# Performance work log

Hardware: AMD Instinct MI355X
Metric: run time of the kernel (lower is better)

Reference implementation:

```python
import jax, jax.numpy as jnp
import numpy as np

N = 50000        # nodes
E = 800000       # edges (avg degree 16)
C_IN = 128
H = 256          # hidden_channels
C_OUT = 128
DEPTH = 4
K = 2            # k_hops -> K+1 = 3 TAGConv weight matrices
L = DEPTH - 1    # residual layers after layer-0 conv
EPS = 1e-5
SLOPE = 0.01     # LeakyReLU default negative slope


def setup_inputs() -> dict:
    key = jax.random.key(0)
    ks = iter(jax.random.split(key, 24))
    s = 0.02
    x = jax.random.normal(next(ks), (N, C_IN), dtype=jnp.float32)
    edge_index = jax.random.randint(next(ks), (2, E), 0, N, dtype=jnp.int64)
    edge_weight = jax.random.uniform(next(ks), (E,), dtype=jnp.float32)
    return {
        'x': x,
        'edge_index': edge_index,
        'edge_weight': edge_weight,
        'W_emb': jax.random.normal(next(ks), (C_IN, H)) * s,
        'b_emb': jnp.zeros((H,), jnp.float32),
        'conv0_W': jax.random.normal(next(ks), (K + 1, H, H)) * s,
        'conv0_b': jnp.zeros((H,), jnp.float32),
        'norm_g': jnp.ones((L, H), jnp.float32),
        'norm_b': jnp.zeros((L, H), jnp.float32),
        'conv_W': jax.random.normal(next(ks), (L, K + 1, H, H)) * s,
        'conv_b': jnp.zeros((L, H), jnp.float32),
        'mlp_W1': jax.random.normal(next(ks), (L, H, 4 * H)) * s,
        'mlp_b1': jnp.zeros((L, 4 * H), jnp.float32),
        'mlp_g': jnp.ones((L, 4 * H), jnp.float32),
        'mlp_bb': jnp.zeros((L, 4 * H), jnp.float32),
        'mlp_W2': jax.random.normal(next(ks), (L, 4 * H, H)) * s,
        'mlp_b2': jnp.zeros((L, H), jnp.float32),
        'W_out': jax.random.normal(next(ks), (H, C_OUT)) * s,
        'b_out': jnp.zeros((C_OUT,), jnp.float32),
    }


def _bn(h, g, b):
    # BatchNorm1d over node dim (training-mode batch statistics)
    m = h.mean(axis=0)
    v = h.var(axis=0)
    return g * (h - m) * jax.lax.rsqrt(v + EPS) + b


def _tagconv(h, src, dst, ew, Ws, b):
    # TAGConv (normalize=False, no self loops): sum_k (A^k h) W_k + b
    out = h @ Ws[0]
    p = h
    for k in range(1, Ws.shape[0]):
        msg = p[src] * ew[:, None]                      # [E, H] gather
        p = jax.ops.segment_sum(msg, dst, num_segments=h.shape[0])
        out = out + p @ Ws[k]
    return out + b


def reference(x, edge_index, edge_weight, W_emb, b_emb, conv0_W, conv0_b,
              norm_g, norm_b, conv_W, conv_b, mlp_W1, mlp_b1, mlp_g, mlp_bb,
              mlp_W2, mlp_b2, W_out, b_out):
    src, dst = edge_index[0], edge_index[1]
    h = x @ W_emb + b_emb                               # x_embed (t=None)
    h = _tagconv(h, src, dst, edge_weight, conv0_W, conv0_b)  # layer-0 conv only
    for l in range(norm_g.shape[0]):                    # res+ blocks
        z = jax.nn.leaky_relu(_bn(h, norm_g[l], norm_b[l]), SLOPE)
        z = _tagconv(z, src, dst, edge_weight, conv_W[l], conv_b[l])
        # pyg MLP [H, 4H, H]: Linear -> BN -> act -> Linear (plain last)
        z = jax.nn.leaky_relu(_bn(z @ mlp_W1[l] + mlp_b1[l], mlp_g[l], mlp_bb[l]), SLOPE)
        z = z @ mlp_W2[l] + mlp_b2[l]
        h = h + z                                       # residual (res=Identity)
    return h @ W_out + b_out
```

## Files before the change

### kernel.cpp

```cpp
#include <hip/hip_runtime.h>

#define HDIM 256
#define EPSV 1e-5f
#define SLOPEV 0.01f

typedef __bf16 bf16;
typedef bf16  bf16x8 __attribute__((ext_vector_type(8)));
typedef bf16  bf16x4 __attribute__((ext_vector_type(4)));
typedef float f32x4  __attribute__((ext_vector_type(4)));

#define GLD16(g, l) __builtin_amdgcn_global_load_lds( \
    (const __attribute__((address_space(1))) void*)(g), \
    (__attribute__((address_space(3))) void*)(l), 16, 0, 0)

template<bool STORE_BF16>
__global__ __launch_bounds__(256)
void gemm_bt_k(const bf16* A0, const bf16* A1, const bf16* A2, const bf16* A3,
               int nseg, int segK,
               const bf16* __restrict__ Wt,
               const float* __restrict__ bias, const bf16* __restrict__ addb,
               void* out0, void* out1, void* out2, void* out3, int ldo,
               int n_store, float* part, int n_stats)
{
    __shared__ char smem[32768];
    bf16* As = (bf16*)smem;
    bf16* Bs = (bf16*)(smem + 16384);

    const int tid = threadIdx.x;
    const int wave = tid >> 6, lane = tid & 63;
    const int quad = lane >> 4, l16 = lane & 15;
    const int waveM = (wave >> 1) * 64, waveN = (wave & 1) * 64;
    const int bm = blockIdx.y * 128, bn = blockIdx.x * 128;
    const int K = nseg * segK;

    const bf16* segs[4] = {A0, A1, A2, A3};
    const int srow = tid >> 3;
    const int skof = (tid & 7) * 8;
    char* lA = (char*)As + wave * 1024;
    char* lB = (char*)Bs + wave * 1024;
    const bf16* pa = As + (waveM + l16) * 64 + quad * 8;
    const bf16* pb = Bs + (waveN + l16) * 64 + quad * 8;

    f32x4 acc[4][4] = {};

    for (int s = 0; s < nseg; ++s) {
        const bf16* gA = segs[s] + (size_t)(bm + srow) * segK + skof;
        const bf16* gB = Wt + (size_t)(bn + srow) * K + s * segK + skof;
        const size_t offA = (size_t)32 * segK;
        const size_t offB = (size_t)32 * K;
        for (int kt = 0; kt < segK; kt += 64) {
            GLD16(gA,            lA);
            GLD16(gA + offA,     lA + 4096);
            GLD16(gA + 2 * offA, lA + 8192);
            GLD16(gA + 3 * offA, lA + 12288);
            GLD16(gB,            lB);
            GLD16(gB + offB,     lB + 4096);
            GLD16(gB + 2 * offB, lB + 8192);
            GLD16(gB + 3 * offB, lB + 12288);
            gA += 64; gB += 64;
            __syncthreads();

#pragma unroll
            for (int ks = 0; ks < 2; ++ks) {
                const bf16* pak = pa + ks * 32;
                const bf16* pbk = pb + ks * 32;
                bf16x8 a0 = *(const bf16x8*)(pak);
                bf16x8 a1 = *(const bf16x8*)(pak + 16 * 64);
                bf16x8 a2 = *(const bf16x8*)(pak + 32 * 64);
                bf16x8 a3 = *(const bf16x8*)(pak + 48 * 64);
                bf16x8 b0 = *(const bf16x8*)(pbk);
                bf16x8 b1 = *(const bf16x8*)(pbk + 16 * 64);
                bf16x8 b2 = *(const bf16x8*)(pbk + 32 * 64);
                bf16x8 b3 = *(const bf16x8*)(pbk + 48 * 64);

                acc[0][0] = __builtin_amdgcn_mfma_f32_16x16x32_bf16(a0, b0, acc[0][0], 0, 0, 0);
                acc[0][1] = __builtin_amdgcn_mfma_f32_16x16x32_bf16(a0, b1, acc[0][1], 0, 0, 0);
                acc[0][2] = __builtin_amdgcn_mfma_f32_16x16x32_bf16(a0, b2, acc[0][2], 0, 0, 0);
                acc[0][3] = __builtin_amdgcn_mfma_f32_16x16x32_bf16(a0, b3, acc[0][3], 0, 0, 0);
                acc[1][0] = __builtin_amdgcn_mfma_f32_16x16x32_bf16(a1, b0, acc[1][0], 0, 0, 0);
                acc[1][1] = __builtin_amdgcn_mfma_f32_16x16x32_bf16(a1, b1, acc[1][1], 0, 0, 0);
                acc[1][2] = __builtin_amdgcn_mfma_f32_16x16x32_bf16(a1, b2, acc[1][2], 0, 0, 0);
                acc[1][3] = __builtin_amdgcn_mfma_f32_16x16x32_bf16(a1, b3, acc[1][3], 0, 0, 0);
                acc[2][0] = __builtin_amdgcn_mfma_f32_16x16x32_bf16(a2, b0, acc[2][0], 0, 0, 0);
                acc[2][1] = __builtin_amdgcn_mfma_f32_16x16x32_bf16(a2, b1, acc[2][1], 0, 0, 0);
                acc[2][2] = __builtin_amdgcn_mfma_f32_16x16x32_bf16(a2, b2, acc[2][2], 0, 0, 0);
                acc[2][3] = __builtin_amdgcn_mfma_f32_16x16x32_bf16(a2, b3, acc[2][3], 0, 0, 0);
                acc[3][0] = __builtin_amdgcn_mfma_f32_16x16x32_bf16(a3, b0, acc[3][0], 0, 0, 0);
                acc[3][1] = __builtin_amdgcn_mfma_f32_16x16x32_bf16(a3, b1, acc[3][1], 0, 0, 0);
                acc[3][2] = __builtin_amdgcn_mfma_f32_16x16x32_bf16(a3, b2, acc[3][2], 0, 0, 0);
                acc[3][3] = __builtin_amdgcn_mfma_f32_16x16x32_bf16(a3, b3, acc[3][3], 0, 0, 0);
            }
            __syncthreads();
        }
    }

    float bv[4];
#pragma unroll
    for (int j = 0; j < 4; ++j)
        bv[j] = bias ? bias[bn + waveN + j * 16 + l16] : 0.f;
#pragma unroll
    for (int i = 0; i < 4; ++i)
#pragma unroll
        for (int j = 0; j < 4; ++j)
#pragma unroll
            for (int r = 0; r < 4; ++r)
                acc[i][j][r] += bv[j];

    void* outs[4] = {out0, out1, out2, out3};

    if (STORE_BF16) {
        char* stg = smem + wave * 4352;
        float s8[8] = {}, q8[8] = {};
        const int rsel = lane >> 3, csel = lane & 7;
#pragma unroll
        for (int ih = 0; ih < 2; ++ih) {
            __syncthreads();
#pragma unroll
            for (int iw = 0; iw < 2; ++iw) {
                int i = ih * 2 + iw;
#pragma unroll
                for (int j = 0; j < 4; ++j)
#pragma unroll
                    for (int r = 0; r < 4; ++r)
                        *(bf16*)(stg + ((iw * 16 + quad * 4 + r) * 68 + j * 16 + l16) * 2)
                            = (bf16)acc[i][j][r];
            }
            __syncthreads();
#pragma unroll
            for (int rr = 0; rr < 4; ++rr) {
                int rl = rsel + rr * 8;
                bf16x4 lo = *(const bf16x4*)(stg + (rl * 68 + csel * 8) * 2);
                bf16x4 hi = *(const bf16x4*)(stg + (rl * 68 + csel * 8 + 4) * 2);
                int rowg = bm + waveM + ih * 32 + rl;
                int colg = bn + waveN + csel * 8;
                int cseg = colg >> 8, cloc = colg & 255;
                size_t idx = (size_t)rowg * ldo + cloc;
                float f[8];
#pragma unroll
                for (int u = 0; u < 4; ++u) { f[u] = (float)lo[u]; f[4 + u] = (float)hi[u]; }
                if (addb) {
                    bf16x8 o = *(const bf16x8*)(addb + idx);
#pragma unroll
                    for (int u = 0; u < 8; ++u) f[u] += (float)o[u];
                }
                bf16x8 w;
#pragma unroll
                for (int u = 0; u < 8; ++u) w[u] = (bf16)f[u];
                if (rowg < n_store) *(bf16x8*)((bf16*)outs[cseg] + idx) = w;
                if (part && rowg < n_stats) {
#pragma unroll
                    for (int u = 0; u < 8; ++u) { s8[u] += f[u]; q8[u] += f[u] * f[u]; }
                }
            }
        }
        if (part) {
#pragma unroll
            for (int m = 8; m <= 32; m <<= 1)
#pragma unroll
                for (int u = 0; u < 8; ++u) {
                    s8[u] += __shfl_xor(s8[u], m, 64);
                    q8[u] += __shfl_xor(q8[u], m, 64);
                }
            __syncthreads();
            float* Ls = (float*)smem;
            float* Lq = Ls + 256;
            if (rsel == 0) {
#pragma unroll
                for (int u = 0; u < 8; ++u) {
                    Ls[wave * 64 + csel * 8 + u] = s8[u];
                    Lq[wave * 64 + csel * 8 + u] = q8[u];
                }
            }
            __syncthreads();
            if (tid < 128) {
                int hi = tid >> 6, c6 = tid & 63;
                float s = Ls[hi * 64 + c6] + Ls[(hi + 2) * 64 + c6];
                float q = Lq[hi * 64 + c6] + Lq[(hi + 2) * 64 + c6];
                int Mtot = gridDim.x * 128;
                int colg = bn + tid;
                part[(size_t)blockIdx.y * Mtot + colg] = s;
                part[(size_t)(gridDim.y + blockIdx.y) * Mtot + colg] = q;
            }
        }
    } else {
#pragma unroll
        for (int i = 0; i < 4; ++i)
#pragma unroll
            for (int j = 0; j < 4; ++j) {
                int colg = bn + waveN + j * 16 + l16;
                int cseg = colg >> 8, cloc = colg & 255;
#pragma unroll
                for (int r = 0; r < 4; ++r) {
                    int rowg = bm + waveM + i * 16 + quad * 4 + r;
                    if (rowg < n_store)
                        ((float*)outs[cseg])[(size_t)rowg * ldo + cloc] = acc[i][j][r];
                }
            }
    }
}

__global__ __launch_bounds__(256)
void finalize_k(const float* __restrict__ part, int GY, int M,
                const float* __restrict__ g, const float* __restrict__ bb,
                float* __restrict__ coef, float invn)
{
    const int c = blockIdx.x;
    const int t = threadIdx.x;
    float s = 0.f, q = 0.f;
    const float* ps = part + c;
    const float* pq = part + (size_t)GY * M + c;
    for (int i = t; i < GY; i += 256) {
        s += ps[(size_t)i * M];
        q += pq[(size_t)i * M];
    }
#pragma unroll
    for (int m = 1; m <= 32; m <<= 1) {
        s += __shfl_xor(s, m, 64);
        q += __shfl_xor(q, m, 64);
    }
    __shared__ float Ls[4], Lq[4];
    const int w = t >> 6, l = t & 63;
    if (l == 0) { Ls[w] = s; Lq[w] = q; }
    __syncthreads();
    if (t == 0) {
        s = Ls[0] + Ls[1] + Ls[2] + Ls[3];
        q = Lq[0] + Lq[1] + Lq[2] + Lq[3];
        float mean = s * invn;
        float var  = q * invn - mean * mean;
        float a = g[c] * rsqrtf(var + EPSV);
        coef[c]     = a;
        coef[M + c] = bb[c] - mean * a;
    }
}

__global__ __launch_bounds__(256)
void transpose_cvt_k(const float* __restrict__ src, bf16* __restrict__ dst,
                     int Kseg, int M, int G)
{
    __shared__ float t[32][33];
    const int z = blockIdx.z;
    src += (size_t)z * Kseg * M;
    const int ldd = G * Kseg;
    dst += (size_t)(z / G) * M * ldd + (size_t)(z % G) * Kseg;
    const int tM = blockIdx.x * 32, tK = blockIdx.y * 32;
    const int tx = threadIdx.x & 31, ty = threadIdx.x >> 5;
#pragma unroll
    for (int r = 0; r < 4; ++r)
        t[ty + r * 8][tx] = src[(size_t)(tK + ty + r * 8) * M + tM + tx];
    __syncthreads();
#pragma unroll
    for (int r = 0; r < 4; ++r)
        dst[(size_t)(tM + ty + r * 8) * ldd + tK + tx] = (bf16)t[tx][ty + r * 8];
}

__global__ __launch_bounds__(256)
void cvt_bf_k(const float* __restrict__ src, bf16* __restrict__ dst, long n4)
{
    long i = (long)blockIdx.x * blockDim.x + threadIdx.x;
    if (i >= n4) return;
    float4 v = ((const float4*)src)[i];
    bf16x4 o; o[0] = (bf16)v.x; o[1] = (bf16)v.y; o[2] = (bf16)v.z; o[3] = (bf16)v.w;
    ((bf16x4*)dst)[i] = o;
}

__global__ __launch_bounds__(256)
void deg_k(const int* __restrict__ dst, int* __restrict__ deg, int E)
{
    int e = blockIdx.x * blockDim.x + threadIdx.x;
    if (e < E) atomicAdd(&deg[dst[e]], 1);
}

__global__ __launch_bounds__(256)
void blocksum_k(const int* __restrict__ deg, int* __restrict__ bsum, int N)
{
    int i = blockIdx.x * 256 + threadIdx.x;
    int v = (i < N) ? deg[i] : 0;
#pragma unroll
    for (int m = 1; m <= 32; m <<= 1) v += __shfl_xor(v, m, 64);
    __shared__ int Ls[4];
    if ((threadIdx.x & 63) == 0) Ls[threadIdx.x >> 6] = v;
    __syncthreads();
    if (threadIdx.x == 0) bsum[blockIdx.x] = Ls[0] + Ls[1] + Ls[2] + Ls[3];
}

__global__ __launch_bounds__(256)
void topscan_k(const int* __restrict__ bsum, int* __restrict__ boff, int nb)
{
    __shared__ int s[256];
    int t = threadIdx.x;
    int v = (t < nb) ? bsum[t] : 0;
    s[t] = v;
    __syncthreads();
    for (int off = 1; off < 256; off <<= 1) {
        int u = (t >= off) ? s[t - off] : 0;
        __syncthreads();
        s[t] += u;
        __syncthreads();
    }
    if (t < nb) boff[t] = s[t] - v;
}

__global__ __launch_bounds__(256)
void scatterscan_k(int* __restrict__ deg_wp, const int* __restrict__ boff,
                   int* __restrict__ rowptr, int N)
{
    __shared__ int s[256];
    int t = threadIdx.x;
    int i = blockIdx.x * 256 + t;
    int v = (i < N) ? deg_wp[i] : 0;
    s[t] = v;
    __syncthreads();
    for (int off = 1; off < 256; off <<= 1) {
        int u = (t >= off) ? s[t - off] : 0;
        __syncthreads();
        s[t] += u;
        __syncthreads();
    }
    if (i < N) {
        int incl = s[t] + boff[blockIdx.x];
        rowptr[i + 1] = incl;
        deg_wp[i] = incl - v;
        if (i == 0) rowptr[0] = 0;
    }
}

__global__ __launch_bounds__(256)
void reorder_k(const int* __restrict__ src, const int* __restrict__ dst,
               const float* __restrict__ ew, int* __restrict__ wp,
               int* __restrict__ col, float* __restrict__ wgt, int E)
{
    int e = blockIdx.x * blockDim.x + threadIdx.x;
    if (e >= E) return;
    int d = dst[e];
    int pos = atomicAdd(&wp[d], 1);
    col[pos] = src[e];
    wgt[pos] = ew[e];
}

__global__ __launch_bounds__(256)
void spmm_pull_k(const bf16* __restrict__ P, const int* __restrict__ rowptr,
                 const int* __restrict__ col, const float* __restrict__ wgt,
                 bf16* __restrict__ Q, int N)
{
    int node = blockIdx.x * 8 + (threadIdx.x >> 5);
    int l = threadIdx.x & 31;
    if (node >= N) return;
    int e = rowptr[node], end = rowptr[node + 1];
    float acc[8] = {};
    for (; e + 1 < end; e += 2) {
        int   s0 = col[e], s1 = col[e + 1];
        float w0 = wgt[e], w1 = wgt[e + 1];
        bf16x8 v0 = *(const bf16x8*)(P + (size_t)s0 * HDIM + l * 8);
        bf16x8 v1 = *(const bf16x8*)(P + (size_t)s1 * HDIM + l * 8);
#pragma unroll
        for (int u = 0; u < 8; ++u)
            acc[u] += (float)v0[u] * w0 + (float)v1[u] * w1;
    }
    if (e < end) {
        int s0 = col[e]; float w0 = wgt[e];
        bf16x8 v0 = *(const bf16x8*)(P + (size_t)s0 * HDIM + l * 8);
#pragma unroll
        for (int u = 0; u < 8; ++u) acc[u] += (float)v0[u] * w0;
    }
    bf16x8 o;
#pragma unroll
    for (int u = 0; u < 8; ++u) o[u] = (bf16)acc[u];
    *(bf16x8*)(Q + (size_t)node * HDIM + l * 8) = o;
}

__global__ __launch_bounds__(256)
void apply_bn_k(const bf16* __restrict__ X, const float* __restrict__ coef,
                bf16* __restrict__ Y, int n)
{
    __shared__ float aL[256], bL[256];
    const int tid = threadIdx.x;
    aL[tid] = coef[tid]; bL[tid] = coef[256 + tid];
    __syncthreads();
    long n4 = (long)n * 64;
    for (long i = (long)blockIdx.x * 256 + tid; i < n4; i += (long)gridDim.x * 256) {
        bf16x4 v = ((const bf16x4*)X)[i];
        int c4 = (int)(i & 63) * 4;
        float r0 = fmaf((float)v[0], aL[c4 + 0], bL[c4 + 0]); r0 = r0 > 0.f ? r0 : SLOPEV * r0;
        float r1 = fmaf((float)v[1], aL[c4 + 1], bL[c4 + 1]); r1 = r1 > 0.f ? r1 : SLOPEV * r1;
        float r2 = fmaf((float)v[2], aL[c4 + 2], bL[c4 + 2]); r2 = r2 > 0.f ? r2 : SLOPEV * r2;
        float r3 = fmaf((float)v[3], aL[c4 + 3], bL[c4 + 3]); r3 = r3 > 0.f ? r3 : SLOPEV * r3;
        bf16x4 o; o[0] = (bf16)r0; o[1] = (bf16)r1; o[2] = (bf16)r2; o[3] = (bf16)r3;
        ((bf16x4*)Y)[i] = o;
    }
}

__global__ __launch_bounds__(256)
void apply_bn4_k(bf16* X0, bf16* X1, bf16* X2, bf16* X3,
                 const float* __restrict__ coef, int n)
{
    __shared__ float aL[1024], bL[1024];
    const int tid = threadIdx.x;
#pragma unroll
    for (int q = 0; q < 4; ++q) {
        int c = q * 256 + tid;
        aL[c] = coef[c]; bL[c] = coef[1024 + c];
    }
    __syncthreads();
    bf16* Xs[4] = {X0, X1, X2, X3};
    long per = (long)n * 64;
    long stride = (long)gridDim.x * 256;
    for (int q = 0; q < 4; ++q) {
        bf16* X = Xs[q];
        int cbase = q * 256;
        for (long i = (long)blockIdx.x * 256 + tid; i < per; i += stride) {
            bf16x4 v = ((const bf16x4*)X)[i];
            int c4 = cbase + (int)(i & 63) * 4;
            float r0 = fmaf((float)v[0], aL[c4 + 0], bL[c4 + 0]); r0 = r0 > 0.f ? r0 : SLOPEV * r0;
            float r1 = fmaf((float)v[1], aL[c4 + 1], bL[c4 + 1]); r1 = r1 > 0.f ? r1 : SLOPEV * r1;
            float r2 = fmaf((float)v[2], aL[c4 + 2], bL[c4 + 2]); r2 = r2 > 0.f ? r2 : SLOPEV * r2;
            float r3 = fmaf((float)v[3], aL[c4 + 3], bL[c4 + 3]); r3 = r3 > 0.f ? r3 : SLOPEV * r3;
            bf16x4 o; o[0] = (bf16)r0; o[1] = (bf16)r1; o[2] = (bf16)r2; o[3] = (bf16)r3;
            ((bf16x4*)X)[i] = o;
        }
    }
}

struct GemmArgs {
    const bf16 *A0, *A1, *A2, *A3; int nseg, segK;
    const bf16* Wt; const float* bias; const bf16* addb;
    void *o0, *o1, *o2, *o3; int ldo, M, n_store;
    float* part; int n_stats;
};

static void gemm(hipStream_t st, const GemmArgs& a, int GY, bool store_bf16)
{
    dim3 g(a.M / 128, GY), b(256);
    if (store_bf16)
        gemm_bt_k<true><<<g, b, 0, st>>>(a.A0, a.A1, a.A2, a.A3, a.nseg, a.segK,
            a.Wt, a.bias, a.addb, a.o0, a.o1, a.o2, a.o3, a.ldo, a.n_store,
            a.part, a.n_stats);
    else
        gemm_bt_k<false><<<g, b, 0, st>>>(a.A0, a.A1, a.A2, a.A3, a.nseg, a.segK,
            a.Wt, a.bias, a.addb, a.o0, a.o1, a.o2, a.o3, a.ldo, a.n_store,
            a.part, a.n_stats);
}

extern "C" void kernel_launch(void* const* d_in, const int* in_sizes, int n_in,
                              void* d_out, int out_size, void* d_ws, size_t ws_size,
                              hipStream_t stream)
{
    const float* x       = (const float*)d_in[0];
    const int*   ei      = (const int*)d_in[1];
    const float* ew      = (const float*)d_in[2];
    const float* W_emb   = (const float*)d_in[3];
    const float* b_emb   = (const float*)d_in[4];
    const float* conv0_W = (const float*)d_in[5];
    const float* conv0_b = (const float*)d_in[6];
    const float* norm_g  = (const float*)d_in[7];
    const float* norm_b  = (const float*)d_in[8];
    const float* conv_W  = (const float*)d_in[9];
    const float* conv_b  = (const float*)d_in[10];
    const float* mlp_W1  = (const float*)d_in[11];
    const float* mlp_b1  = (const float*)d_in[12];
    const float* mlp_g   = (const float*)d_in[13];
    const float* mlp_bb  = (const float*)d_in[14];
    const float* mlp_W2  = (const float*)d_in[15];
    const float* mlp_b2  = (const float*)d_in[16];
    const float* W_out   = (const float*)d_in[17];
    const float* b_out   = (const float*)d_in[18];

    const int N = in_sizes[0] / 128;
    const int E = in_sizes[2];
    const int* srcI = ei;
    const int* dstI = ei + E;
    const int N_pad = ((N + 127) / 128) * 128;
    const int GY = N_pad / 128;
    const int NB = (N + 255) / 256;

    const size_t NHp = (size_t)N_pad * HDIM;
    bf16* xb = (bf16*)d_ws;
    bf16* hb = xb + (size_t)N_pad * 128;
    bf16* cb = hb + NHp;
    bf16* p1 = cb + NHp;
    bf16* p2 = p1 + NHp;
    bf16* e1 = p2 + NHp;
    bf16* e2 = e1 + NHp;
    bf16* wa = e2 + NHp;
    bf16* Wt_emb   = wa;
    bf16* Wt_conv0 = wa + 32768;
    bf16* Wt_conv  = wa + 229376;
    bf16* Wt_mlp1  = wa + 819200;
    bf16* Wt_mlp2  = wa + 1605632;
    bf16* Wt_out   = wa + 2392064;
    float* cf_h   = (float*)(wa + 2424832);
    float* cf_m   = cf_h + 512;
    float* partb  = cf_m + 2048;
    int*   rowptr = (int*)(partb + 2 * (size_t)GY * 1024);
    int*   wp     = rowptr + (N + 1);
    int*   col    = wp + N;
    float* wgt    = (float*)(col + E);
    int*   bsum   = (int*)(wgt + E);
    int*   boff   = bsum + 256;

    const float invn = 1.0f / (float)N;
    dim3 pg((N + 7) / 8), pb(256);

    hipMemsetAsync(wp, 0, (size_t)N * 4, stream);
    deg_k<<<dim3((E + 255) / 256), dim3(256), 0, stream>>>(dstI, wp, E);
    blocksum_k<<<dim3(NB), dim3(256), 0, stream>>>(wp, bsum, N);
    topscan_k<<<dim3(1), dim3(256), 0, stream>>>(bsum, boff, NB);
    scatterscan_k<<<dim3(NB), dim3(256), 0, stream>>>(wp, boff, rowptr, N);
    reorder_k<<<dim3((E + 255) / 256), dim3(256), 0, stream>>>(srcI, dstI, ew, wp, col, wgt, E);

    cvt_bf_k<<<dim3((N * 32 + 255) / 256), dim3(256), 0, stream>>>(x, xb, (long)N * 32);
    transpose_cvt_k<<<dim3(8, 4, 1), dim3(256), 0, stream>>>(W_emb, Wt_emb, 128, 256, 1);
    transpose_cvt_k<<<dim3(8, 8, 3), dim3(256), 0, stream>>>(conv0_W, Wt_conv0, 256, 256, 3);
    transpose_cvt_k<<<dim3(8, 8, 9), dim3(256), 0, stream>>>(conv_W, Wt_conv, 256, 256, 3);
    transpose_cvt_k<<<dim3(32, 8, 3), dim3(256), 0, stream>>>(mlp_W1, Wt_mlp1, 256, 1024, 1);
    transpose_cvt_k<<<dim3(8, 32, 3), dim3(256), 0, stream>>>(mlp_W2, Wt_mlp2, 1024, 256, 1);
    transpose_cvt_k<<<dim3(4, 8, 1), dim3(256), 0, stream>>>(W_out, Wt_out, 256, 128, 1);

    {
        GemmArgs a{xb, xb, xb, xb, 1, 128, Wt_emb, b_emb, nullptr,
                   cb, cb, cb, cb, HDIM, 256, N_pad, nullptr, 0};
        gemm(stream, a, GY, true);
    }

    spmm_pull_k<<<pg, pb, 0, stream>>>(cb, rowptr, col, wgt, p1, N);
    spmm_pull_k<<<pg, pb, 0, stream>>>(p1, rowptr, col, wgt, p2, N);
    {
        GemmArgs a{cb, p1, p2, p2, 3, 256, Wt_conv0, conv0_b, nullptr,
                   hb, hb, hb, hb, HDIM, 256, N_pad, partb, N};
        gemm(stream, a, GY, true);
    }
    finalize_k<<<dim3(256), dim3(256), 0, stream>>>(partb, GY, 256, norm_g, norm_b, cf_h, invn);

    for (int l = 0; l < 3; ++l) {
        apply_bn_k<<<dim3(1024), dim3(256), 0, stream>>>(hb, cf_h, e1, N);

        spmm_pull_k<<<pg, pb, 0, stream>>>(e1, rowptr, col, wgt, p1, N);
        spmm_pull_k<<<pg, pb, 0, stream>>>(p1, rowptr, col, wgt, p2, N);
        {
            GemmArgs a{e1, p1, p2, p2, 3, 256, Wt_conv + (size_t)l * 196608,
                       conv_b + l * 256, nullptr, cb, cb, cb, cb, HDIM, 256, N_pad,
                       nullptr, 0};
            gemm(stream, a, GY, true);
        }

        {
            GemmArgs a{cb, cb, cb, cb, 1, 256, Wt_mlp1 + (size_t)l * 262144,
                       mlp_b1 + (size_t)l * 1024, nullptr, p1, p2, e1, e2, HDIM, 1024,
                       N_pad, partb, N};
            gemm(stream, a, GY, true);
        }
        finalize_k<<<dim3(1024), dim3(256), 0, stream>>>(partb, GY, 1024,
                                                         mlp_g + (size_t)l * 1024,
                                                         mlp_bb + (size_t)l * 1024, cf_m, invn);

        apply_bn4_k<<<dim3(2048), dim3(256), 0, stream>>>(p1, p2, e1, e2, cf_m, N);

        {
            GemmArgs a{p1, p2, e1, e2, 4, 256, Wt_mlp2 + (size_t)l * 262144,
                       mlp_b2 + l * 256, hb, hb, hb, hb, hb, HDIM, 256, N_pad,
                       (l < 2) ? partb : nullptr, N};
            gemm(stream, a, GY, true);
        }
        if (l < 2)
            finalize_k<<<dim3(256), dim3(256), 0, stream>>>(partb, GY, 256,
                                                            norm_g + (l + 1) * 256,
                                                            norm_b + (l + 1) * 256, cf_h, invn);
    }

    {
        GemmArgs a{hb, hb, hb, hb, 1, 256, Wt_out, b_out, nullptr,
                   d_out, d_out, d_out, d_out, 128, 128, N, nullptr, 0};
        gemm(stream, a, GY, false);
    }
}
```

Before: 1.494 ms.

## Double-buffer GEMM LDS tiles with K=32 steps and XCD-aware block remap

Restructures the GEMM main loop from a single-buffered K=64 tile into a double-buffered K=32 pipeline. The next tile's global-to-LDS loads are issued before computing on the current one, and each iteration has one barrier instead of two. Blocks are also remapped so consecutive tiles land on the same XCD chiplet for better L2 reuse. The intent is to hide load latency behind MFMA work, at the cost of smaller per-iteration compute and more loop overhead.

Measured after the change: 1.394 ms. -6.7%, faster.

```diff
diff --git a/kernel.cpp b/kernel.cpp
--- a/kernel.cpp
+++ b/kernel.cpp
@@ -23,75 +23,85 @@
                int n_store, float* part, int n_stats)
 {
     __shared__ char smem[32768];
-    bf16* As = (bf16*)smem;
-    bf16* Bs = (bf16*)(smem + 16384);
 
     const int tid = threadIdx.x;
     const int wave = tid >> 6, lane = tid & 63;
     const int quad = lane >> 4, l16 = lane & 15;
     const int waveM = (wave >> 1) * 64, waveN = (wave & 1) * 64;
-    const int bm = blockIdx.y * 128, bn = blockIdx.x * 128;
+
+    int bid = blockIdx.y * gridDim.x + blockIdx.x;
+    const int nwg = gridDim.x * gridDim.y;
+    if ((nwg & 7) == 0) {
+        const int cpx = nwg >> 3;
+        bid = (bid & 7) * cpx + (bid >> 3);
+    }
+    const int bx = bid % gridDim.x, by = bid / gridDim.x;
+    const int bm = by * 128, bn = bx * 128;
     const int K = nseg * segK;
 
     const bf16* segs[4] = {A0, A1, A2, A3};
-    const int srow = tid >> 3;
-    const int skof = (tid & 7) * 8;
-    char* lA = (char*)As + wave * 1024;
-    char* lB = (char*)Bs + wave * 1024;
-    const bf16* pa = As + (waveM + l16) * 64 + quad * 8;
-    const bf16* pb = Bs + (waveN + l16) * 64 + quad * 8;
+    const int srow = tid >> 2;
+    const int skof = (tid & 3) * 8;
+    char* lAw = smem + wave * 1024;
+    char* lBw = smem + 16384 + wave * 1024;
 
     f32x4 acc[4][4] = {};
 
-    for (int s = 0; s < nseg; ++s) {
-        const bf16* gA = segs[s] + (size_t)(bm + srow) * segK + skof;
-        const bf16* gB = Wt + (size_t)(bn + srow) * K + s * segK + skof;
-        const size_t offA = (size_t)32 * segK;
-        const size_t offB = (size_t)32 * K;
-        for (int kt = 0; kt < segK; kt += 64) {
-            GLD16(gA,            lA);
-            GLD16(gA + offA,     lA + 4096);
-            GLD16(gA + 2 * offA, lA + 8192);
-            GLD16(gA + 3 * offA, lA + 12288);
-            GLD16(gB,            lB);
-            GLD16(gB + offB,     lB + 4096);
-            GLD16(gB + 2 * offB, lB + 8192);
-            GLD16(gB + 3 * offB, lB + 12288);
-            gA += 64; gB += 64;
-            __syncthreads();
-
-#pragma unroll
-            for (int ks = 0; ks < 2; ++ks) {
-                const bf16* pak = pa + ks * 32;
-                const bf16* pbk = pb + ks * 32;
-                bf16x8 a0 = *(const bf16x8*)(pak);
-                bf16x8 a1 = *(const bf16x8*)(pak + 16 * 64);
-                bf16x8 a2 = *(const bf16x8*)(pak + 32 * 64);
-                bf16x8 a3 = *(const bf16x8*)(pak + 48 * 64);
-                bf16x8 b0 = *(const bf16x8*)(pbk);
-                bf16x8 b1 = *(const bf16x8*)(pbk + 16 * 64);
-                bf16x8 b2 = *(const bf16x8*)(pbk + 32 * 64);
-                bf16x8 b3 = *(const bf16x8*)(pbk + 48 * 64);
-
-                acc[0][0] = __builtin_amdgcn_mfma_f32_16x16x32_bf16(a0, b0, acc[0][0], 0, 0, 0);
-                acc[0][1] = __builtin_amdgcn_mfma_f32_16x16x32_bf16(a0, b1, acc[0][1], 0, 0, 0);
-                acc[0][2] = __builtin_amdgcn_mfma_f32_16x16x32_bf16(a0, b2, acc[0][2], 0, 0, 0);
-                acc[0][3] = __builtin_amdgcn_mfma_f32_16x16x32_bf16(a0, b3, acc[0][3], 0, 0, 0);
-                acc[1][0] = __builtin_amdgcn_mfma_f32_16x16x32_bf16(a1, b0, acc[1][0], 0, 0, 0);
-                acc[1][1] = __builtin_amdgcn_mfma_f32_16x16x32_bf16(a1, b1, acc[1][1], 0, 0, 0);
-                acc[1][2] = __builtin_amdgcn_mfma_f32_16x16x32_bf16(a1, b2, acc[1][2], 0, 0, 0);
-                acc[1][3] = __builtin_amdgcn_mfma_f32_16x16x32_bf16(a1, b3, acc[1][3], 0, 0, 0);
-                acc[2][0] = __builtin_amdgcn_mfma_f32_16x16x32_bf16(a2, b0, acc[2][0], 0, 0, 0);
-                acc[2][1] = __builtin_amdgcn_mfma_f32_16x16x32_bf16(a2, b1, acc[2][1], 0, 0, 0);
-                acc[2][2] = __builtin_amdgcn_mfma_f32_16x16x32_bf16(a2, b2, acc[2][2], 0, 0, 0);
-                acc[2][3] = __builtin_amdgcn_mfma_f32_16x16x32_bf16(a2, b3, acc[2][3], 0, 0, 0);
-                acc[3][0] = __builtin_amdgcn_mfma_f32_16x16x32_bf16(a3, b0, acc[3][0], 0, 0, 0);
-                acc[3][1] = __builtin_amdgcn_mfma_f32_16x16x32_bf16(a3, b1, acc[3][1], 0, 0, 0);
-                acc[3][2] = __builtin_amdgcn_mfma_f32_16x16x32_bf16(a3, b2, acc[3][2], 0, 0, 0);
-                acc[3][3] = __builtin_amdgcn_mfma_f32_16x16x32_bf16(a3, b3, acc[3][3], 0, 0, 0);
-            }
-            __syncthreads();
-        }
+    const int spseg = segK >> 5;
+    const int T = nseg * spseg;
+
+    auto stage = [&](int s, int kt, int b) {
+        const bf16* gA = segs[s] + (size_t)(bm + srow) * segK + kt + skof;
+        const bf16* gB = Wt + (size_t)(bn + srow) * K + s * segK + kt + skof;
+        char* lA = lAw + b * 8192;
+        char* lB = lBw + b * 8192;
+        GLD16(gA,                     lA);
+        GLD16(gA + (size_t)64 * segK, lA + 4096);
+        GLD16(gB,                     lB);
+        GLD16(gB + (size_t)64 * K,    lB + 4096);
+    };
+
+    stage(0, 0, 0);
+    __syncthreads();
+
+    int s = 0, kt = 0;
+    for (int t = 0; t < T; ++t) {
+        int s2 = s, kt2 = kt + 32;
+        if (kt2 == segK) { s2++; kt2 = 0; }
+        if (t + 1 < T) stage(s2, kt2, (t + 1) & 1);
+
+        const bf16* pa = (const bf16*)(smem + (t & 1) * 8192)
+                         + (waveM + l16) * 32 + quad * 8;
+        const bf16* pb = (const bf16*)(smem + 16384 + (t & 1) * 8192)
+                         + (waveN + l16) * 32 + quad * 8;
+        bf16x8 a0 = *(const bf16x8*)(pa);
+        bf16x8 a1 = *(const bf16x8*)(pa + 16 * 32);
+        bf16x8 a2 = *(const bf16x8*)(pa + 32 * 32);
+        bf16x8 a3 = *(const bf16x8*)(pa + 48 * 32);
+        bf16x8 b0 = *(const bf16x8*)(pb);
+        bf16x8 b1 = *(const bf16x8*)(pb + 16 * 32);
+        bf16x8 b2 = *(const bf16x8*)(pb + 32 * 32);
+        bf16x8 b3 = *(const bf16x8*)(pb + 48 * 32);
+
+        acc[0][0] = __builtin_amdgcn_mfma_f32_16x16x32_bf16(a0, b0, acc[0][0], 0, 0, 0);
+        acc[0][1] = __builtin_amdgcn_mfma_f32_16x16x32_bf16(a0, b1, acc[0][1], 0, 0, 0);
+        acc[0][2] = __builtin_amdgcn_mfma_f32_16x16x32_bf16(a0, b2, acc[0][2], 0, 0, 0);
+        acc[0][3] = __builtin_amdgcn_mfma_f32_16x16x32_bf16(a0, b3, acc[0][3], 0, 0, 0);
+        acc[1][0] = __builtin_amdgcn_mfma_f32_16x16x32_bf16(a1, b0, acc[1][0], 0, 0, 0);
+        acc[1][1] = __builtin_amdgcn_mfma_f32_16x16x32_bf16(a1, b1, acc[1][1], 0, 0, 0);
+        acc[1][2] = __builtin_amdgcn_mfma_f32_16x16x32_bf16(a1, b2, acc[1][2], 0, 0, 0);
+        acc[1][3] = __builtin_amdgcn_mfma_f32_16x16x32_bf16(a1, b3, acc[1][3], 0, 0, 0);
+        acc[2][0] = __builtin_amdgcn_mfma_f32_16x16x32_bf16(a2, b0, acc[2][0], 0, 0, 0);
+        acc[2][1] = __builtin_amdgcn_mfma_f32_16x16x32_bf16(a2, b1, acc[2][1], 0, 0, 0);
+        acc[2][2] = __builtin_amdgcn_mfma_f32_16x16x32_bf16(a2, b2, acc[2][2], 0, 0, 0);
+        acc[2][3] = __builtin_amdgcn_mfma_f32_16x16x32_bf16(a2, b3, acc[2][3], 0, 0, 0);
+        acc[3][0] = __builtin_amdgcn_mfma_f32_16x16x32_bf16(a3, b0, acc[3][0], 0, 0, 0);
+        acc[3][1] = __builtin_amdgcn_mfma_f32_16x16x32_bf16(a3, b1, acc[3][1], 0, 0, 0);
+        acc[3][2] = __builtin_amdgcn_mfma_f32_16x16x32_bf16(a3, b2, acc[3][2], 0, 0, 0);
+        acc[3][3] = __builtin_amdgcn_mfma_f32_16x16x32_bf16(a3, b3, acc[3][3], 0, 0, 0);
+
+        __syncthreads();
+        s = s2; kt = kt2;
     }
 
     float bv[4];
@@ -174,12 +184,12 @@
             __syncthreads();
             if (tid < 128) {
                 int hi = tid >> 6, c6 = tid & 63;
-                float s = Ls[hi * 64 + c6] + Ls[(hi + 2) * 64 + c6];
-                float q = Lq[hi * 64 + c6] + Lq[(hi + 2) * 64 + c6];
+                float sv = Ls[hi * 64 + c6] + Ls[(hi + 2) * 64 + c6];
+                float qv = Lq[hi * 64 + c6] + Lq[(hi + 2) * 64 + c6];
                 int Mtot = gridDim.x * 128;
                 int colg = bn + tid;
-                part[(size_t)blockIdx.y * Mtot + colg] = s;
-                part[(size_t)(gridDim.y + blockIdx.y) * Mtot + colg] = q;
+                part[(size_t)by * Mtot + colg] = sv;
+                part[(size_t)(gridDim.y + by) * Mtot + colg] = qv;
             }
         }
     } else {
```
